# Performance work log

Measured on AMD Instinct MI355X. Metric: run time of the kernel, lower is better.

Reference implementation:

```python
import jax, jax.numpy as jnp
import numpy as np

N, D, V = 2048, 64, 2048


def setup_inputs() -> dict:
    key = jax.random.key(0)
    k_ids, k_emb, k_tree, k_map = jax.random.split(key, 4)
    language_ids = jax.random.randint(k_ids, (N,), 0, V)
    language_embeddings = jax.random.normal(k_emb, (N, D), dtype=jnp.float32)
    # symmetric distance tables, mimicking the symmetric try/except dict lookup
    t = jax.random.uniform(k_tree, (V, V), dtype=jnp.float32)
    tree_dist = (t + t.T) * 0.5
    m = jax.random.uniform(k_map, (V, V), dtype=jnp.float32)
    map_dist = (m + m.T) * 0.5
    return {
        "language_ids": language_ids,
        "language_embeddings": language_embeddings,
        "tree_dist": tree_dist,
        "map_dist": map_dist,
    }


def reference(language_ids, language_embeddings, tree_dist, map_dist):
    # pairwise mean-L1 distance between embeddings: [N, N]
    emb_dist = jnp.mean(
        jnp.abs(language_embeddings[:, None, :] - language_embeddings[None, :, :]),
        axis=-1,
    )
    # largest_value_map_dist as computed in __init__
    largest = jnp.max(map_dist)
    ii = language_ids[:, None]  # [N, 1]
    jj = language_ids[None, :]  # [1, N]
    metric = (tree_dist[ii, jj] + map_dist[ii, jj] / largest) * 0.5  # [N, N]
    # pairs with equal language ids are skipped in the original loop
    mask = (ii != jj).astype(emb_dist.dtype)
    per_pair = jnp.abs(emb_dist - metric) * mask
    return jnp.sum(per_pair) / jnp.sum(mask)
```

## Files before the change

### kernel.cpp

```cpp
#include <hip/hip_runtime.h>
#include <hip/hip_bf16.h>

#define NL 2048
#define DE 64
#define VV 2048
#define BT 64
#define NT (NL / BT)
#define NBLK (NT * (NT + 1) / 2)
#define STT 68


__global__ __launch_bounds__(1024) void prep_kernel(const int* __restrict__ ids,
                                                    const float4* __restrict__ m4,
                                                    float* __restrict__ pmax,
                                                    int* __restrict__ perm,
                                                    int* __restrict__ sids) {
    const int t = threadIdx.x;
    const int lane = t & 63, wave = t >> 6;
    const int b = blockIdx.x;

    if (b < 256) {
        const float4* p = m4 + (size_t)b * 4096;
        const float4 x0 = p[t], x1 = p[t + 1024], x2 = p[t + 2048], x3 = p[t + 3072];
        float v = fmaxf(fmaxf(fmaxf(x0.x, x0.y), fmaxf(x0.z, x0.w)),
                        fmaxf(fmaxf(x1.x, x1.y), fmaxf(x1.z, x1.w)));
        v = fmaxf(v, fmaxf(fmaxf(x2.x, x2.y), fmaxf(x2.z, x2.w)));
        v = fmaxf(v, fmaxf(fmaxf(x3.x, x3.y), fmaxf(x3.z, x3.w)));
        #pragma unroll
        for (int o = 32; o > 0; o >>= 1)
            v = fmaxf(v, __shfl_down(v, o));
        __shared__ float wl[16];
        if (lane == 0) wl[wave] = v;
        __syncthreads();
        if (t == 0) {
            float m = wl[0];
            #pragma unroll
            for (int i = 1; i < 16; ++i) m = fmaxf(m, wl[i]);
            pmax[b] = m;
        }
    } else {
        __shared__ unsigned hist[VV];
        __shared__ unsigned offs[VV];
        __shared__ unsigned wtot[16];
        __shared__ unsigned wexc[16];
        hist[2 * t] = 0u; hist[2 * t + 1] = 0u;
        __syncthreads();
        const int id0 = ids[2 * t], id1 = ids[2 * t + 1];
        atomicAdd(&hist[id0], 1u);
        atomicAdd(&hist[id1], 1u);
        __syncthreads();
        const unsigned h0 = hist[2 * t], h1 = hist[2 * t + 1];
        const unsigned s = h0 + h1;
        unsigned ps = s;
        #pragma unroll
        for (int o = 1; o < 64; o <<= 1) {
            unsigned u = __shfl_up(ps, o);
            if (lane >= o) ps += u;
        }
        if (lane == 63) wtot[wave] = ps;
        __syncthreads();
        if (wave == 0 && lane < 16) {
            unsigned v = wtot[lane];
            unsigned pv = v;
            #pragma unroll
            for (int o = 1; o < 16; o <<= 1) {
                unsigned u = __shfl_up(pv, o);
                if (lane >= o) pv += u;
            }
            wexc[lane] = pv - v;
        }
        __syncthreads();
        const unsigned ex = wexc[wave] + ps - s;
        offs[2 * t]     = ex;
        offs[2 * t + 1] = ex + h0;
        __syncthreads();
        unsigned p0 = atomicAdd(&offs[id0], 1u);
        perm[p0] = 2 * t;     sids[p0] = id0;
        unsigned p1 = atomicAdd(&offs[id1], 1u);
        perm[p1] = 2 * t + 1; sids[p1] = id1;
    }
}

__global__ __launch_bounds__(256) void loss_kernel(
    const float* __restrict__ emb,
    const float* __restrict__ tree, const float* __restrict__ mapd,
    const int* __restrict__ perm, const int* __restrict__ sids,
    const float* __restrict__ pmax,
    float* __restrict__ psum, unsigned* __restrict__ pcnt)
{
    const int t = threadIdx.x;

    const int L = blockIdx.x;
    int bi = (int)((65.0f - sqrtf(4225.0f - 8.0f * (float)L)) * 0.5f);
    if (bi > NT - 1) bi = NT - 1;
    if (bi < 0) bi = 0;
    while (NT * bi - bi * (bi - 1) / 2 > L) --bi;
    while (NT * (bi + 1) - (bi + 1) * bi / 2 <= L) ++bi;
    const int bj = bi + (L - (NT * bi - bi * (bi - 1) / 2));

    __shared__ __align__(16) float Eit[DE][STT];
    __shared__ __align__(16) float Ejt[DE][STT];
    __shared__ int idi[BT];
    __shared__ int idj[BT];
    __shared__ float wm[4];

    float pv = pmax[t];

    {
        const int r  = t & 63;
        const int c0 = (t >> 6) << 4;
        const int gi = perm[bi * BT + r];
        const int gj = perm[bj * BT + r];
        const float4* pa = (const float4*)(emb + (size_t)gi * DE + c0);
        const float4* pb = (const float4*)(emb + (size_t)gj * DE + c0);
        float4 a0 = pa[0], a1 = pa[1], a2 = pa[2], a3 = pa[3];
        float4 b0 = pb[0], b1 = pb[1], b2 = pb[2], b3 = pb[3];
        Eit[c0 + 0][r]  = a0.x; Eit[c0 + 1][r]  = a0.y; Eit[c0 + 2][r]  = a0.z; Eit[c0 + 3][r]  = a0.w;
        Eit[c0 + 4][r]  = a1.x; Eit[c0 + 5][r]  = a1.y; Eit[c0 + 6][r]  = a1.z; Eit[c0 + 7][r]  = a1.w;
        Eit[c0 + 8][r]  = a2.x; Eit[c0 + 9][r]  = a2.y; Eit[c0 + 10][r] = a2.z; Eit[c0 + 11][r] = a2.w;
        Eit[c0 + 12][r] = a3.x; Eit[c0 + 13][r] = a3.y; Eit[c0 + 14][r] = a3.z; Eit[c0 + 15][r] = a3.w;
        Ejt[c0 + 0][r]  = b0.x; Ejt[c0 + 1][r]  = b0.y; Ejt[c0 + 2][r]  = b0.z; Ejt[c0 + 3][r]  = b0.w;
        Ejt[c0 + 4][r]  = b1.x; Ejt[c0 + 5][r]  = b1.y; Ejt[c0 + 6][r]  = b1.z; Ejt[c0 + 7][r]  = b1.w;
        Ejt[c0 + 8][r]  = b2.x; Ejt[c0 + 9][r]  = b2.y; Ejt[c0 + 10][r] = b2.z; Ejt[c0 + 11][r] = b2.w;
        Ejt[c0 + 12][r] = b3.x; Ejt[c0 + 13][r] = b3.y; Ejt[c0 + 14][r] = b3.z; Ejt[c0 + 15][r] = b3.w;
        if (t < BT)          idi[t] = sids[bi * BT + t];
        else if (t < 2 * BT) idj[t - BT] = sids[bj * BT + (t - BT)];
    }
    #pragma unroll
    for (int o = 32; o > 0; o >>= 1)
        pv = fmaxf(pv, __shfl_down(pv, o));
    if ((t & 63) == 0) wm[t >> 6] = pv;
    __syncthreads();

    const float inv = 1.0f / fmaxf(fmaxf(wm[0], wm[1]), fmaxf(wm[2], wm[3]));

    const int i0 = (t >> 4) * 4;
    const int j0 = (t & 15) * 4;

    float acc[4][4];
    #pragma unroll
    for (int s = 0; s < 4; ++s)
        #pragma unroll
        for (int c = 0; c < 4; ++c) acc[s][c] = 0.0f;

    #pragma unroll 2
    for (int k = 0; k < 16; ++k) {
        #pragma unroll
        for (int q = 0; q < 4; ++q) {
            const int d = 4 * k + q;
            const float4 a = *(const float4*)&Eit[d][i0];
            const float4 b = *(const float4*)&Ejt[d][j0];
            acc[0][0] += fabsf(a.x - b.x); acc[0][1] += fabsf(a.x - b.y);
            acc[0][2] += fabsf(a.x - b.z); acc[0][3] += fabsf(a.x - b.w);
            acc[1][0] += fabsf(a.y - b.x); acc[1][1] += fabsf(a.y - b.y);
            acc[1][2] += fabsf(a.y - b.z); acc[1][3] += fabsf(a.y - b.w);
            acc[2][0] += fabsf(a.z - b.x); acc[2][1] += fabsf(a.z - b.y);
            acc[2][2] += fabsf(a.z - b.z); acc[2][3] += fabsf(a.z - b.w);
            acc[3][0] += fabsf(a.w - b.x); acc[3][1] += fabsf(a.w - b.y);
            acc[3][2] += fabsf(a.w - b.z); acc[3][3] += fabsf(a.w - b.w);
        }
    }

    float pp = 0.0f;
    unsigned cnt = 0;
    #pragma unroll
    for (int s = 0; s < 4; ++s) {
        const int ia = idi[i0 + s];
        #pragma unroll
        for (int c = 0; c < 4; ++c) {
            const int ja = idj[j0 + c];
            const int off = ia * VV + ja;
            const float metric = (tree[off] + mapd[off] * inv) * 0.5f;
            if (ia != ja) {
                pp += fabsf(acc[s][c] * (1.0f / (float)DE) - metric);
                cnt += 1u;
            }
        }
    }

    #pragma unroll
    for (int o = 32; o > 0; o >>= 1) {
        pp  += __shfl_down(pp, o);
        cnt += __shfl_down(cnt, o);
    }
    __shared__ float    wsum_l[4];
    __shared__ unsigned wcnt_l[4];
    if ((t & 63) == 0) { wsum_l[t >> 6] = pp; wcnt_l[t >> 6] = cnt; }
    __syncthreads();
    if (t == 0) {
        const float    w = (bi == bj) ? 1.0f : 2.0f;
        const unsigned u = (bi == bj) ? 1u : 2u;
        psum[L] = (wsum_l[0] + wsum_l[1] + wsum_l[2] + wsum_l[3]) * w;
        pcnt[L] = (wcnt_l[0] + wcnt_l[1] + wcnt_l[2] + wcnt_l[3]) * u;
    }
}

__global__ __launch_bounds__(1024) void finalize_kernel(const float* __restrict__ psum,
                                                        const unsigned* __restrict__ pcnt,
                                                        float* __restrict__ out) {
    const int t = threadIdx.x;
    const int lane = t & 63, wave = t >> 6;
    double s = 0.0;
    unsigned c = 0;
    if (t < NBLK) { s = (double)psum[t]; c = pcnt[t]; }
    #pragma unroll
    for (int o = 32; o > 0; o >>= 1) {
        s += __shfl_down(s, o);
        c += __shfl_down(c, o);
    }
    __shared__ double   sl[16];
    __shared__ unsigned cl[16];
    if (lane == 0) { sl[wave] = s; cl[wave] = c; }
    __syncthreads();
    if (t == 0) {
        double   S = sl[0];
        unsigned C = cl[0];
        #pragma unroll
        for (int i = 1; i < 16; ++i) { S += sl[i]; C += cl[i]; }
        out[0] = (float)(S / (double)C);
    }
}

extern "C" void kernel_launch(void* const* d_in, const int* in_sizes, int n_in,
                              void* d_out, int out_size, void* d_ws, size_t ws_size,
                              hipStream_t stream) {
    const int*   ids  = (const int*)d_in[0];
    const float* emb  = (const float*)d_in[1];
    const float* tree = (const float*)d_in[2];
    const float* mapd = (const float*)d_in[3];
    float* out = (float*)d_out;

    float*    pmax = (float*)d_ws;
    int*      perm = (int*)((char*)d_ws + 1024);
    int*      sids = (int*)((char*)d_ws + 9216);
    float*    psum = (float*)((char*)d_ws + 17408);
    unsigned* pcnt = (unsigned*)((char*)d_ws + 19520);

    prep_kernel<<<257, 1024, 0, stream>>>(ids, (const float4*)mapd, pmax, perm, sids);

    loss_kernel<<<NBLK, 256, 0, stream>>>(emb, tree, mapd, perm, sids, pmax, psum, pcnt);

    finalize_kernel<<<1, 1024, 0, stream>>>(psum, pcnt, out);
}
```

Before: 103.1 us.

## Fuse prep, loss and finalize into one cooperative kernel with grid syncs

Merges the three kernels (map max reduction plus id counting sort, pairwise loss tiles, final reduction) into a single cooperative launch of 528 blocks separated by grid.sync. The map max is now spread across 527 blocks and the sort runs in the last block with 256 threads, sharing one union of LDS. This is meant to remove two kernel launch gaps and launch overhead. In exchange it adds grid-wide barrier cost and requires all 528 blocks to be co-resident, which is plausible on a 256-CU part.

```diff
diff --git a/kernel.cpp b/kernel.cpp
--- a/kernel.cpp
+++ b/kernel.cpp
@@ -1,5 +1,7 @@
 #include <hip/hip_runtime.h>
 #include <hip/hip_bf16.h>
+#include <hip/hip_cooperative_groups.h>
+namespace cg = cooperative_groups;
 
 #define NL 2048
 #define DE 64
@@ -10,87 +12,110 @@
 #define STT 68
 
 
-__global__ __launch_bounds__(1024) void prep_kernel(const int* __restrict__ ids,
-                                                    const float4* __restrict__ m4,
-                                                    float* __restrict__ pmax,
-                                                    int* __restrict__ perm,
-                                                    int* __restrict__ sids) {
+union SharedU {
+    struct {
+        float Eit[DE][STT];
+        float Ejt[DE][STT];
+        int   idi[BT];
+        int   idj[BT];
+        float wm[4];
+        float    wsum_l[4];
+        unsigned wcnt_l[4];
+    } loss;
+    struct {
+        unsigned hist[VV];
+        unsigned offs[VV];
+        unsigned wtot[4];
+        unsigned wexc[4];
+    } sort;
+    struct {
+        float wl[4];
+    } mx;
+    struct {
+        double   sl[4];
+        unsigned cl[4];
+    } fin;
+};
+
+__global__ __launch_bounds__(256) void fused_kernel(
+    const int* __restrict__ ids, const float* __restrict__ emb,
+    const float* __restrict__ tree, const float* __restrict__ mapd,
+    float* __restrict__ pmax, int* __restrict__ perm, int* __restrict__ sids,
+    float* __restrict__ psum, unsigned* __restrict__ pcnt,
+    float* __restrict__ out)
+{
+    __shared__ SharedU sh;
+    cg::grid_group grid = cg::this_grid();
+
     const int t = threadIdx.x;
     const int lane = t & 63, wave = t >> 6;
-    const int b = blockIdx.x;
-
-    if (b < 256) {
-        const float4* p = m4 + (size_t)b * 4096;
-        const float4 x0 = p[t], x1 = p[t + 1024], x2 = p[t + 2048], x3 = p[t + 3072];
-        float v = fmaxf(fmaxf(fmaxf(x0.x, x0.y), fmaxf(x0.z, x0.w)),
-                        fmaxf(fmaxf(x1.x, x1.y), fmaxf(x1.z, x1.w)));
-        v = fmaxf(v, fmaxf(fmaxf(x2.x, x2.y), fmaxf(x2.z, x2.w)));
-        v = fmaxf(v, fmaxf(fmaxf(x3.x, x3.y), fmaxf(x3.z, x3.w)));
+    const int L = blockIdx.x;
+
+    if (L < NBLK - 1) {
+        const float4* m4 = (const float4*)mapd;
+        const int n4 = (VV * VV) / 4;
+        float v = 0.0f;
+        for (int i = L * 256 + t; i < n4; i += (NBLK - 1) * 256) {
+            float4 x = m4[i];
+            v = fmaxf(v, fmaxf(fmaxf(x.x, x.y), fmaxf(x.z, x.w)));
+        }
         #pragma unroll
         for (int o = 32; o > 0; o >>= 1)
             v = fmaxf(v, __shfl_down(v, o));
-        __shared__ float wl[16];
-        if (lane == 0) wl[wave] = v;
+        if (lane == 0) sh.mx.wl[wave] = v;
         __syncthreads();
         if (t == 0) {
-            float m = wl[0];
-            #pragma unroll
-            for (int i = 1; i < 16; ++i) m = fmaxf(m, wl[i]);
-            pmax[b] = m;
+            float m = fmaxf(fmaxf(sh.mx.wl[0], sh.mx.wl[1]), fmaxf(sh.mx.wl[2], sh.mx.wl[3]));
+            pmax[L] = m;
         }
     } else {
-        __shared__ unsigned hist[VV];
-        __shared__ unsigned offs[VV];
-        __shared__ unsigned wtot[16];
-        __shared__ unsigned wexc[16];
-        hist[2 * t] = 0u; hist[2 * t + 1] = 0u;
-        __syncthreads();
-        const int id0 = ids[2 * t], id1 = ids[2 * t + 1];
-        atomicAdd(&hist[id0], 1u);
-        atomicAdd(&hist[id1], 1u);
-        __syncthreads();
-        const unsigned h0 = hist[2 * t], h1 = hist[2 * t + 1];
-        const unsigned s = h0 + h1;
+        #pragma unroll
+        for (int k = 0; k < 8; ++k) sh.sort.hist[t * 8 + k] = 0u;
+        __syncthreads();
+        int myid[8];
+        #pragma unroll
+        for (int k = 0; k < 8; ++k) {
+            myid[k] = ids[t * 8 + k];
+            atomicAdd(&sh.sort.hist[myid[k]], 1u);
+        }
+        __syncthreads();
+        unsigned loc[8], s = 0;
+        #pragma unroll
+        for (int k = 0; k < 8; ++k) { loc[k] = sh.sort.hist[t * 8 + k]; s += loc[k]; }
         unsigned ps = s;
         #pragma unroll
         for (int o = 1; o < 64; o <<= 1) {
             unsigned u = __shfl_up(ps, o);
             if (lane >= o) ps += u;
         }
-        if (lane == 63) wtot[wave] = ps;
-        __syncthreads();
-        if (wave == 0 && lane < 16) {
-            unsigned v = wtot[lane];
+        if (lane == 63) sh.sort.wtot[wave] = ps;
+        __syncthreads();
+        if (wave == 0 && lane < 4) {
+            unsigned v = sh.sort.wtot[lane];
             unsigned pv = v;
             #pragma unroll
-            for (int o = 1; o < 16; o <<= 1) {
+            for (int o = 1; o < 4; o <<= 1) {
                 unsigned u = __shfl_up(pv, o);
                 if (lane >= o) pv += u;
             }
-            wexc[lane] = pv - v;
-        }
-        __syncthreads();
-        const unsigned ex = wexc[wave] + ps - s;
-        offs[2 * t]     = ex;
-        offs[2 * t + 1] = ex + h0;
-        __syncthreads();
-        unsigned p0 = atomicAdd(&offs[id0], 1u);
-        perm[p0] = 2 * t;     sids[p0] = id0;
-        unsigned p1 = atomicAdd(&offs[id1], 1u);
-        perm[p1] = 2 * t + 1; sids[p1] = id1;
-    }
-}
-
-__global__ __launch_bounds__(256) void loss_kernel(
-    const float* __restrict__ emb,
-    const float* __restrict__ tree, const float* __restrict__ mapd,
-    const int* __restrict__ perm, const int* __restrict__ sids,
-    const float* __restrict__ pmax,
-    float* __restrict__ psum, unsigned* __restrict__ pcnt)
-{
-    const int t = threadIdx.x;
-
-    const int L = blockIdx.x;
+            sh.sort.wexc[lane] = pv - v;
+        }
+        __syncthreads();
+        unsigned ex = sh.sort.wexc[wave] + ps - s;
+        #pragma unroll
+        for (int k = 0; k < 8; ++k) { sh.sort.offs[t * 8 + k] = ex; ex += loc[k]; }
+        __syncthreads();
+        #pragma unroll
+        for (int k = 0; k < 8; ++k) {
+            unsigned p = atomicAdd(&sh.sort.offs[myid[k]], 1u);
+            perm[p] = t * 8 + k;
+            sids[p] = myid[k];
+        }
+        if (t == 0) pmax[NBLK - 1] = 0.0f;
+    }
+
+    grid.sync();
+
     int bi = (int)((65.0f - sqrtf(4225.0f - 8.0f * (float)L)) * 0.5f);
     if (bi > NT - 1) bi = NT - 1;
     if (bi < 0) bi = 0;
@@ -98,13 +123,8 @@
     while (NT * (bi + 1) - (bi + 1) * bi / 2 <= L) ++bi;
     const int bj = bi + (L - (NT * bi - bi * (bi - 1) / 2));
 
-    __shared__ __align__(16) float Eit[DE][STT];
-    __shared__ __align__(16) float Ejt[DE][STT];
-    __shared__ int idi[BT];
-    __shared__ int idj[BT];
-    __shared__ float wm[4];
-
-    float pv = pmax[t];
+    float pv = fmaxf(pmax[t], pmax[t + 256]);
+    if (t < NBLK - 512) pv = fmaxf(pv, pmax[t + 512]);
 
     {
         const int r  = t & 63;
@@ -115,24 +135,33 @@
         const float4* pb = (const float4*)(emb + (size_t)gj * DE + c0);
         float4 a0 = pa[0], a1 = pa[1], a2 = pa[2], a3 = pa[3];
         float4 b0 = pb[0], b1 = pb[1], b2 = pb[2], b3 = pb[3];
-        Eit[c0 + 0][r]  = a0.x; Eit[c0 + 1][r]  = a0.y; Eit[c0 + 2][r]  = a0.z; Eit[c0 + 3][r]  = a0.w;
-        Eit[c0 + 4][r]  = a1.x; Eit[c0 + 5][r]  = a1.y; Eit[c0 + 6][r]  = a1.z; Eit[c0 + 7][r]  = a1.w;
-        Eit[c0 + 8][r]  = a2.x; Eit[c0 + 9][r]  = a2.y; Eit[c0 + 10][r] = a2.z; Eit[c0 + 11][r] = a2.w;
-        Eit[c0 + 12][r] = a3.x; Eit[c0 + 13][r] = a3.y; Eit[c0 + 14][r] = a3.z; Eit[c0 + 15][r] = a3.w;
-        Ejt[c0 + 0][r]  = b0.x; Ejt[c0 + 1][r]  = b0.y; Ejt[c0 + 2][r]  = b0.z; Ejt[c0 + 3][r]  = b0.w;
-        Ejt[c0 + 4][r]  = b1.x; Ejt[c0 + 5][r]  = b1.y; Ejt[c0 + 6][r]  = b1.z; Ejt[c0 + 7][r]  = b1.w;
-        Ejt[c0 + 8][r]  = b2.x; Ejt[c0 + 9][r]  = b2.y; Ejt[c0 + 10][r] = b2.z; Ejt[c0 + 11][r] = b2.w;
-        Ejt[c0 + 12][r] = b3.x; Ejt[c0 + 13][r] = b3.y; Ejt[c0 + 14][r] = b3.z; Ejt[c0 + 15][r] = b3.w;
-        if (t < BT)          idi[t] = sids[bi * BT + t];
-        else if (t < 2 * BT) idj[t - BT] = sids[bj * BT + (t - BT)];
+        sh.loss.Eit[c0 + 0][r]  = a0.x; sh.loss.Eit[c0 + 1][r]  = a0.y;
+        sh.loss.Eit[c0 + 2][r]  = a0.z; sh.loss.Eit[c0 + 3][r]  = a0.w;
+        sh.loss.Eit[c0 + 4][r]  = a1.x; sh.loss.Eit[c0 + 5][r]  = a1.y;
+        sh.loss.Eit[c0 + 6][r]  = a1.z; sh.loss.Eit[c0 + 7][r]  = a1.w;
+        sh.loss.Eit[c0 + 8][r]  = a2.x; sh.loss.Eit[c0 + 9][r]  = a2.y;
+        sh.loss.Eit[c0 + 10][r] = a2.z; sh.loss.Eit[c0 + 11][r] = a2.w;
+        sh.loss.Eit[c0 + 12][r] = a3.x; sh.loss.Eit[c0 + 13][r] = a3.y;
+        sh.loss.Eit[c0 + 14][r] = a3.z; sh.loss.Eit[c0 + 15][r] = a3.w;
+        sh.loss.Ejt[c0 + 0][r]  = b0.x; sh.loss.Ejt[c0 + 1][r]  = b0.y;
+        sh.loss.Ejt[c0 + 2][r]  = b0.z; sh.loss.Ejt[c0 + 3][r]  = b0.w;
+        sh.loss.Ejt[c0 + 4][r]  = b1.x; sh.loss.Ejt[c0 + 5][r]  = b1.y;
+        sh.loss.Ejt[c0 + 6][r]  = b1.z; sh.loss.Ejt[c0 + 7][r]  = b1.w;
+        sh.loss.Ejt[c0 + 8][r]  = b2.x; sh.loss.Ejt[c0 + 9][r]  = b2.y;
+        sh.loss.Ejt[c0 + 10][r] = b2.z; sh.loss.Ejt[c0 + 11][r] = b2.w;
+        sh.loss.Ejt[c0 + 12][r] = b3.x; sh.loss.Ejt[c0 + 13][r] = b3.y;
+        sh.loss.Ejt[c0 + 14][r] = b3.z; sh.loss.Ejt[c0 + 15][r] = b3.w;
+        if (t < BT)          sh.loss.idi[t] = sids[bi * BT + t];
+        else if (t < 2 * BT) sh.loss.idj[t - BT] = sids[bj * BT + (t - BT)];
     }
     #pragma unroll
     for (int o = 32; o > 0; o >>= 1)
         pv = fmaxf(pv, __shfl_down(pv, o));
-    if ((t & 63) == 0) wm[t >> 6] = pv;
+    if (lane == 0) sh.loss.wm[wave] = pv;
     __syncthreads();
 
-    const float inv = 1.0f / fmaxf(fmaxf(wm[0], wm[1]), fmaxf(wm[2], wm[3]));
+    const float inv = 1.0f / fmaxf(fmaxf(sh.loss.wm[0], sh.loss.wm[1]),
+                                   fmaxf(sh.loss.wm[2], sh.loss.wm[3]));
 
     const int i0 = (t >> 4) * 4;
     const int j0 = (t & 15) * 4;
@@ -148,8 +177,8 @@
         #pragma unroll
         for (int q = 0; q < 4; ++q) {
             const int d = 4 * k + q;
-            const float4 a = *(const float4*)&Eit[d][i0];
-            const float4 b = *(const float4*)&Ejt[d][j0];
+            const float4 a = *(const float4*)&sh.loss.Eit[d][i0];
+            const float4 b = *(const float4*)&sh.loss.Ejt[d][j0];
             acc[0][0] += fabsf(a.x - b.x); acc[0][1] += fabsf(a.x - b.y);
             acc[0][2] += fabsf(a.x - b.z); acc[0][3] += fabsf(a.x - b.w);
             acc[1][0] += fabsf(a.y - b.x); acc[1][1] += fabsf(a.y - b.y);
@@ -165,10 +194,10 @@
     unsigned cnt = 0;
     #pragma unroll
     for (int s = 0; s < 4; ++s) {
-        const int ia = idi[i0 + s];
+        const int ia = sh.loss.idi[i0 + s];
         #pragma unroll
         for (int c = 0; c < 4; ++c) {
-            const int ja = idj[j0 + c];
+            const int ja = sh.loss.idj[j0 + c];
             const int off = ia * VV + ja;
             const float metric = (tree[off] + mapd[off] * inv) * 0.5f;
             if (ia != ja) {
@@ -183,41 +212,35 @@
         pp  += __shfl_down(pp, o);
         cnt += __shfl_down(cnt, o);
     }
-    __shared__ float    wsum_l[4];
-    __shared__ unsigned wcnt_l[4];
-    if ((t & 63) == 0) { wsum_l[t >> 6] = pp; wcnt_l[t >> 6] = cnt; }
+    if (lane == 0) { sh.loss.wsum_l[wave] = pp; sh.loss.wcnt_l[wave] = cnt; }
     __syncthreads();
     if (t == 0) {
         const float    w = (bi == bj) ? 1.0f : 2.0f;
         const unsigned u = (bi == bj) ? 1u : 2u;
-        psum[L] = (wsum_l[0] + wsum_l[1] + wsum_l[2] + wsum_l[3]) * w;
-        pcnt[L] = (wcnt_l[0] + wcnt_l[1] + wcnt_l[2] + wcnt_l[3]) * u;
-    }
-}
-
-__global__ __launch_bounds__(1024) void finalize_kernel(const float* __restrict__ psum,
-                                                        const unsigned* __restrict__ pcnt,
-                                                        float* __restrict__ out) {
-    const int t = threadIdx.x;
-    const int lane = t & 63, wave = t >> 6;
-    double s = 0.0;
-    unsigned c = 0;
-    if (t < NBLK) { s = (double)psum[t]; c = pcnt[t]; }
-    #pragma unroll
-    for (int o = 32; o > 0; o >>= 1) {
-        s += __shfl_down(s, o);
-        c += __shfl_down(c, o);
-    }
-    __shared__ double   sl[16];
-    __shared__ unsigned cl[16];
-    if (lane == 0) { sl[wave] = s; cl[wave] = c; }
-    __syncthreads();
-    if (t == 0) {
-        double   S = sl[0];
-        unsigned C = cl[0];
-        #pragma unroll
-        for (int i = 1; i < 16; ++i) { S += sl[i]; C += cl[i]; }
-        out[0] = (float)(S / (double)C);
+        psum[L] = (sh.loss.wsum_l[0] + sh.loss.wsum_l[1] +
+                   sh.loss.wsum_l[2] + sh.loss.wsum_l[3]) * w;
+        pcnt[L] = (sh.loss.wcnt_l[0] + sh.loss.wcnt_l[1] +
+                   sh.loss.wcnt_l[2] + sh.loss.wcnt_l[3]) * u;
+    }
+
+    grid.sync();
+
+    if (L == 0) {
+        double   s = (double)psum[t] + (double)psum[t + 256];
+        unsigned c = pcnt[t] + pcnt[t + 256];
+        if (t < NBLK - 512) { s += (double)psum[t + 512]; c += pcnt[t + 512]; }
+        #pragma unroll
+        for (int o = 32; o > 0; o >>= 1) {
+            s += __shfl_down(s, o);
+            c += __shfl_down(c, o);
+        }
+        if (lane == 0) { sh.fin.sl[wave] = s; sh.fin.cl[wave] = c; }
+        __syncthreads();
+        if (t == 0) {
+            double   S = sh.fin.sl[0] + sh.fin.sl[1] + sh.fin.sl[2] + sh.fin.sl[3];
+            unsigned C = sh.fin.cl[0] + sh.fin.cl[1] + sh.fin.cl[2] + sh.fin.cl[3];
+            out[0] = (float)(S / (double)C);
+        }
     }
 }
 
@@ -231,14 +254,14 @@
     float* out = (float*)d_out;
 
     float*    pmax = (float*)d_ws;
-    int*      perm = (int*)((char*)d_ws + 1024);
-    int*      sids = (int*)((char*)d_ws + 9216);
-    float*    psum = (float*)((char*)d_ws + 17408);
-    unsigned* pcnt = (unsigned*)((char*)d_ws + 19520);
-
-    prep_kernel<<<257, 1024, 0, stream>>>(ids, (const float4*)mapd, pmax, perm, sids);
-
-    loss_kernel<<<NBLK, 256, 0, stream>>>(emb, tree, mapd, perm, sids, pmax, psum, pcnt);
-
-    finalize_kernel<<<1, 1024, 0, stream>>>(psum, pcnt, out);
+    float*    psum = (float*)((char*)d_ws + 4096);
+    unsigned* pcnt = (unsigned*)((char*)d_ws + 8192);
+    int*      perm = (int*)((char*)d_ws + 12288);
+    int*      sids = (int*)((char*)d_ws + 20480);
+
+    void* args[] = { (void*)&ids, (void*)&emb, (void*)&tree, (void*)&mapd,
+                     (void*)&pmax, (void*)&perm, (void*)&sids,
+                     (void*)&psum, (void*)&pcnt, (void*)&out };
+    hipLaunchCooperativeKernel((void*)fused_kernel, dim3(NBLK), dim3(256),
+                               args, 0, stream);
 }
```

Result: slower. 215.9 us (+109.3%).
